# Optimization experiments

Hardware: AMD Instinct MI355X
Metric: run time of the kernel (lower is better)

Reference implementation:

```python
import jax, jax.numpy as jnp
import numpy as np

D_MODEL = 1024
N_HEADS = 16
HEAD_DIM = D_MODEL // N_HEADS
SCALE = HEAD_DIM ** -0.5
BATCH = 4
SEQ = 2048


def setup_inputs() -> dict:
    key = jax.random.key(0)
    k_x, k_wqkv, k_bqkv, k_wo, k_bo = jax.random.split(key, 5)
    x = jax.random.normal(k_x, (BATCH, SEQ, D_MODEL), dtype=jnp.float32)
    # causal mask: True = masked (matches torch masked_fill semantics)
    mask = jnp.triu(jnp.ones((SEQ, SEQ), dtype=bool), k=1)
    # Linear params (stored as [in, out] for x @ W)
    lim_qkv = (1.0 / D_MODEL) ** 0.5
    W_qkv = jax.random.uniform(k_wqkv, (D_MODEL, 3 * D_MODEL), jnp.float32, -lim_qkv, lim_qkv)
    b_qkv = jax.random.uniform(k_bqkv, (3 * D_MODEL,), jnp.float32, -lim_qkv, lim_qkv)
    W_out = jax.random.uniform(k_wo, (D_MODEL, D_MODEL), jnp.float32, -lim_qkv, lim_qkv)
    b_out = jax.random.uniform(k_bo, (D_MODEL,), jnp.float32, -lim_qkv, lim_qkv)
    return {"x": x, "mask": mask, "W_qkv": W_qkv, "b_qkv": b_qkv, "W_out": W_out, "b_out": b_out}


def reference(x, mask, W_qkv, b_qkv, W_out, b_out):
    b, s, d = x.shape
    qkv = x @ W_qkv + b_qkv                      # [b, s, 3d]
    qkv = qkv.reshape(b, s, 3, N_HEADS, HEAD_DIM)
    qkv = jnp.transpose(qkv, (2, 0, 3, 1, 4))    # [3, b, h, s, hd]
    q, k, v = qkv[0], qkv[1], qkv[2]
    scores = jnp.einsum('bhqd,bhkd->bhqk', q, k) * SCALE  # [b, h, s, s]
    scores = jnp.where(mask[None, None, :, :], -jnp.inf, scores)
    weights = jax.nn.softmax(scores, axis=-1)
    out = jnp.einsum('bhqk,bhkd->bhqd', weights, v)       # [b, h, s, hd]
    out = jnp.transpose(out, (0, 2, 1, 3)).reshape(b, s, d)
    return out @ W_out + b_out
```

## Files before the change

kernel.cpp:

```cpp
#include <hip/hip_runtime.h>

#define BATCH 4
#define SEQ 2048
#define DM 1024
#define NH 16
#define SCALE 0.125f

typedef unsigned short ushort_t;
typedef short bf16x8 __attribute__((ext_vector_type(8)));
typedef float f32x4 __attribute__((ext_vector_type(4)));

__device__ __forceinline__ ushort_t f2bf(float f) {
    unsigned u = __float_as_uint(f);
    unsigned r = (u + 0x7FFFu + ((u >> 16) & 1u)) >> 16;
    return (ushort_t)r;
}

__device__ __forceinline__ unsigned cvtpk_bf16(float lo, float hi) {
    unsigned r;
    asm("v_cvt_pk_bf16_f32 %0, %1, %2" : "=v"(r) : "v"(lo), "v"(hi));
    return r;
}

__device__ __forceinline__ void glds16(const ushort_t* g, ushort_t* l) {
    __builtin_amdgcn_global_load_lds(
        (const __attribute__((address_space(1))) unsigned*)g,
        (__attribute__((address_space(3))) unsigned*)l, 16, 0, 0);
}

__global__ void cast_f32_bf16(const float* __restrict__ in, ushort_t* __restrict__ out, int n) {
    int i = (blockIdx.x * blockDim.x + threadIdx.x) * 4;
    if (i < n) {
        float4 v = *(const float4*)(in + i);
        ushort4 o;
        o.x = f2bf(v.x); o.y = f2bf(v.y); o.z = f2bf(v.z); o.w = f2bf(v.w);
        *(ushort4*)(out + i) = o;
    }
}

__global__ void transpose_cast(const float* __restrict__ in, ushort_t* __restrict__ out,
                               int K, int N) {
    __shared__ float tile[32][33];
    int n0 = blockIdx.x * 32, k0 = blockIdx.y * 32;
    int x = threadIdx.x, y = threadIdx.y;
#pragma unroll
    for (int j = 0; j < 32; j += 8)
        tile[y + j][x] = in[(size_t)(k0 + y + j) * N + n0 + x];
    __syncthreads();
#pragma unroll
    for (int j = 0; j < 32; j += 8)
        out[(size_t)(n0 + y + j) * K + k0 + x] = f2bf(tile[x][y + j]);
}


__global__ __launch_bounds__(256) void gemm_qkv(
    const ushort_t* __restrict__ A, const ushort_t* __restrict__ Bt,
    const float* __restrict__ bias, ushort_t* __restrict__ qk,
    ushort_t* __restrict__ vt, int M, int N, int K) {
    __shared__ __attribute__((aligned(16))) ushort_t As[128 * 64];
    __shared__ __attribute__((aligned(16))) ushort_t Bs[128 * 64];
    const int tid = threadIdx.x;
    const int lane = tid & 63, wave = tid >> 6;
    const int l15 = lane & 15, l4 = lane >> 4;
    const int m0 = blockIdx.y * 128, n0 = blockIdx.x * 128;
    const int wr = (wave >> 1) * 64, wc = (wave & 1) * 64;
    const int r8 = lane >> 3;
    const int kch = (lane & 7) ^ r8;
    const ushort_t* gA = A + (size_t)(m0 + wave * 32 + r8) * K + kch * 8;
    const ushort_t* gB = Bt + (size_t)(n0 + wave * 32 + r8) * K + kch * 8;
    const int r7 = l15 & 7;

    f32x4 acc[4][4];
#pragma unroll
    for (int i = 0; i < 4; ++i)
#pragma unroll
        for (int j = 0; j < 4; ++j) acc[i][j] = (f32x4){0.f, 0.f, 0.f, 0.f};

    for (int k0 = 0; k0 < K; k0 += 64) {
#pragma unroll
        for (int c = 0; c < 4; ++c) {
            glds16(gA + k0 + (size_t)(c * 8) * K, &As[(wave * 32 + c * 8) * 64]);
            glds16(gB + k0 + (size_t)(c * 8) * K, &Bs[(wave * 32 + c * 8) * 64]);
        }
        __syncthreads();
#pragma unroll
        for (int kh = 0; kh < 2; ++kh) {
            const int ch = ((kh * 4 + l4) ^ r7) * 8;
            bf16x8 a[4], b[4];
#pragma unroll
            for (int i = 0; i < 4; ++i) {
                a[i] = *(const bf16x8*)&As[(wr + i * 16 + l15) * 64 + ch];
                b[i] = *(const bf16x8*)&Bs[(wc + i * 16 + l15) * 64 + ch];
            }
#pragma unroll
            for (int mi = 0; mi < 4; ++mi)
#pragma unroll
                for (int ni = 0; ni < 4; ++ni)
                    acc[mi][ni] = __builtin_amdgcn_mfma_f32_16x16x32_bf16(
                        a[mi], b[ni], acc[mi][ni], 0, 0, 0);
        }
        __syncthreads();
    }

    if (n0 < 2048) {
#pragma unroll
        for (int mi = 0; mi < 4; ++mi)
#pragma unroll
            for (int ni = 0; ni < 4; ++ni) {
                const int col = n0 + wc + ni * 16 + l15;
                const float bv = bias[col];
#pragma unroll
                for (int r = 0; r < 4; ++r) {
                    const int row = m0 + wr + mi * 16 + l4 * 4 + r;
                    qk[(size_t)row * 2048 + col] = f2bf(acc[mi][ni][r] + bv);
                }
            }
    } else {
#pragma unroll
        for (int mi = 0; mi < 4; ++mi)
#pragma unroll
            for (int ni = 0; ni < 4; ++ni) {
                const int hdg = n0 + wc + ni * 16 + l15 - 2048;
                const float bv = bias[2048 + hdg];
                const int row0 = m0 + wr + mi * 16 + l4 * 4;
                const int bb = row0 >> 11, s0 = row0 & 2047;
                ushort4 pk;
                pk.x = f2bf(acc[mi][ni][0] + bv);
                pk.y = f2bf(acc[mi][ni][1] + bv);
                pk.z = f2bf(acc[mi][ni][2] + bv);
                pk.w = f2bf(acc[mi][ni][3] + bv);
                *(ushort4*)&vt[((size_t)bb * 1024 + hdg) * 2048 + s0] = pk;
            }
    }
}

__global__ __launch_bounds__(256) void gemm_abt(
    const ushort_t* __restrict__ A, const ushort_t* __restrict__ Bt,
    const float* __restrict__ bias, float* __restrict__ Cout,
    int M, int N, int K) {
    __shared__ __attribute__((aligned(16))) ushort_t As[128 * 64];
    __shared__ __attribute__((aligned(16))) ushort_t Bs[128 * 64];
    const int tid = threadIdx.x;
    const int lane = tid & 63, wave = tid >> 6;
    const int l15 = lane & 15, l4 = lane >> 4;
    const int m0 = blockIdx.y * 128, n0 = blockIdx.x * 128;
    const int wr = (wave >> 1) * 64, wc = (wave & 1) * 64;
    const int r8 = lane >> 3;
    const int kch = (lane & 7) ^ r8;
    const ushort_t* gA = A + (size_t)(m0 + wave * 32 + r8) * K + kch * 8;
    const ushort_t* gB = Bt + (size_t)(n0 + wave * 32 + r8) * K + kch * 8;
    const int r7 = l15 & 7;

    f32x4 acc[4][4];
#pragma unroll
    for (int i = 0; i < 4; ++i)
#pragma unroll
        for (int j = 0; j < 4; ++j) acc[i][j] = (f32x4){0.f, 0.f, 0.f, 0.f};

    for (int k0 = 0; k0 < K; k0 += 64) {
#pragma unroll
        for (int c = 0; c < 4; ++c) {
            glds16(gA + k0 + (size_t)(c * 8) * K, &As[(wave * 32 + c * 8) * 64]);
            glds16(gB + k0 + (size_t)(c * 8) * K, &Bs[(wave * 32 + c * 8) * 64]);
        }
        __syncthreads();
#pragma unroll
        for (int kh = 0; kh < 2; ++kh) {
            const int ch = ((kh * 4 + l4) ^ r7) * 8;
            bf16x8 a[4], b[4];
#pragma unroll
            for (int i = 0; i < 4; ++i) {
                a[i] = *(const bf16x8*)&As[(wr + i * 16 + l15) * 64 + ch];
                b[i] = *(const bf16x8*)&Bs[(wc + i * 16 + l15) * 64 + ch];
            }
#pragma unroll
            for (int mi = 0; mi < 4; ++mi)
#pragma unroll
                for (int ni = 0; ni < 4; ++ni)
                    acc[mi][ni] = __builtin_amdgcn_mfma_f32_16x16x32_bf16(
                        a[mi], b[ni], acc[mi][ni], 0, 0, 0);
        }
        __syncthreads();
    }

#pragma unroll
    for (int mi = 0; mi < 4; ++mi)
#pragma unroll
        for (int ni = 0; ni < 4; ++ni)
#pragma unroll
            for (int r = 0; r < 4; ++r) {
                const int row = m0 + wr + mi * 16 + l4 * 4 + r;
                const int col = n0 + wc + ni * 16 + l15;
                Cout[(size_t)row * N + col] = acc[mi][ni][r] + bias[col];
            }
}

struct AState {
    bf16x8 q0, q1;
    f32x4 o[4];
    float m, l;
};

#define EXPC 0.18033688011112042f

template <bool MASK>
__device__ __forceinline__ void attn_tile(AState& S, const ushort_t* __restrict__ Ks,
                                          const ushort_t* __restrict__ Vt,
                                          ushort_t* __restrict__ Plw,
                                          int l15, int l4, int rel) {
    float p[16];
    float pmax = -INFINITY;
    __builtin_amdgcn_s_setprio(1);
#pragma unroll
    for (int kt = 0; kt < 4; ++kt) {
        const int row = kt * 16 + l15, r7 = row & 7;
        bf16x8 ak0 = *(const bf16x8*)&Ks[row * 64 + ((l4 ^ r7) * 8)];
        bf16x8 ak1 = *(const bf16x8*)&Ks[row * 64 + (((4 + l4) ^ r7) * 8)];
        f32x4 z = {0.f, 0.f, 0.f, 0.f};
        z = __builtin_amdgcn_mfma_f32_16x16x32_bf16(ak0, S.q0, z, 0, 0, 0);
        z = __builtin_amdgcn_mfma_f32_16x16x32_bf16(ak1, S.q1, z, 0, 0, 0);
#pragma unroll
        for (int r = 0; r < 4; ++r) {
            float v = z[r];
            if (MASK) v = (kt * 16 + l4 * 4 + r > rel) ? -INFINITY : v;
            p[kt * 4 + r] = v;
            pmax = fmaxf(pmax, v);
        }
    }
    __builtin_amdgcn_s_setprio(0);
    pmax = fmaxf(pmax, __shfl_xor(pmax, 16));
    pmax = fmaxf(pmax, __shfl_xor(pmax, 32));

    const bool defer = __all(pmax - S.m <= 64.f);
    const float mref = defer ? S.m : fmaxf(S.m, pmax);
    const float mC = mref * EXPC;
    float rsum = 0.f;
#pragma unroll
    for (int i = 0; i < 16; ++i) {
        p[i] = __builtin_exp2f(fmaf(p[i], EXPC, -mC));
        rsum += p[i];
    }
    rsum += __shfl_xor(rsum, 16);
    rsum += __shfl_xor(rsum, 32);
    if (defer) {
        S.l += rsum;
    } else {
        const float scl = __builtin_exp2f((S.m - mref) * EXPC);
        S.l = S.l * scl + rsum;
        S.m = mref;
        const float sc0 = __shfl(scl, l4 * 4 + 0);
        const float sc1 = __shfl(scl, l4 * 4 + 1);
        const float sc2 = __shfl(scl, l4 * 4 + 2);
        const float sc3 = __shfl(scl, l4 * 4 + 3);
#pragma unroll
        for (int dt = 0; dt < 4; ++dt) {
            S.o[dt][0] *= sc0; S.o[dt][1] *= sc1; S.o[dt][2] *= sc2; S.o[dt][3] *= sc3;
        }
    }

    const int pr7 = l15 & 7;
#pragma unroll
    for (int kt = 0; kt < 4; ++kt) {
        uint2 w;
        w.x = cvtpk_bf16(p[kt * 4 + 0], p[kt * 4 + 1]);
        w.y = cvtpk_bf16(p[kt * 4 + 2], p[kt * 4 + 3]);
        *(uint2*)&Plw[l15 * 64 + ((kt * 16 + l4 * 4) ^ (pr7 << 3))] = w;
    }

    bf16x8 pa0 = *(const bf16x8*)&Plw[l15 * 64 + ((l4 ^ pr7) * 8)];
    bf16x8 pa1 = *(const bf16x8*)&Plw[l15 * 64 + (((4 + l4) ^ pr7) * 8)];
    __builtin_amdgcn_s_setprio(1);
#pragma unroll
    for (int dt = 0; dt < 4; ++dt) {
        const int d = dt * 16 + l15, r7 = d & 7;
        bf16x8 bv0 = *(const bf16x8*)&Vt[d * 64 + ((l4 ^ r7) * 8)];
        bf16x8 bv1 = *(const bf16x8*)&Vt[d * 64 + (((4 + l4) ^ r7) * 8)];
        S.o[dt] = __builtin_amdgcn_mfma_f32_16x16x32_bf16(pa0, bv0, S.o[dt], 0, 0, 0);
        S.o[dt] = __builtin_amdgcn_mfma_f32_16x16x32_bf16(pa1, bv1, S.o[dt], 0, 0, 0);
    }
    __builtin_amdgcn_s_setprio(0);
}

__device__ __forceinline__ void process_qblock(
    int bq, const ushort_t* __restrict__ qk, ushort_t* __restrict__ out,
    size_t rowbase, int h, int wave, int l15, int l4,
    const ushort_t* gk, const ushort_t* gvt,
    ushort_t* Ks0, ushort_t* Ks1, ushort_t* Vt0, ushort_t* Vt1, ushort_t* Plw) {
    const int qbase = bq * 64 + wave * 16;

    AState S;
    {
        const ushort_t* qp = qk + (rowbase + qbase + l15) * 2048 + h * 64 + l4 * 8;
        S.q0 = *(const bf16x8*)qp;
        S.q1 = *(const bf16x8*)(qp + 32);
    }
#pragma unroll
    for (int i = 0; i < 4; ++i) S.o[i] = (f32x4){0.f, 0.f, 0.f, 0.f};
    S.m = -INFINITY;
    S.l = 0.f;

    glds16(gk, &Ks0[(wave * 16) * 64]);
    glds16(gk + (size_t)8 * 2048, &Ks0[(wave * 16 + 8) * 64]);
    glds16(gvt, &Vt0[(wave * 16) * 64]);
    glds16(gvt + (size_t)8 * 2048, &Vt0[(wave * 16 + 8) * 64]);
    __syncthreads();

    const int nt = bq + 1;
    for (int t = 0; t < nt; ++t) {
        ushort_t* Kc = (t & 1) ? Ks1 : Ks0;
        ushort_t* Vc = (t & 1) ? Vt1 : Vt0;
        ushort_t* Kn = (t & 1) ? Ks0 : Ks1;
        ushort_t* Vn = (t & 1) ? Vt0 : Vt1;
        if (t + 1 < nt) {
            const size_t koff = (size_t)(t + 1) * 64 * 2048;
            glds16(gk + koff, &Kn[(wave * 16) * 64]);
            glds16(gk + koff + (size_t)8 * 2048, &Kn[(wave * 16 + 8) * 64]);
            const size_t voff = (size_t)(t + 1) * 64;
            glds16(gvt + voff, &Vn[(wave * 16) * 64]);
            glds16(gvt + voff + (size_t)8 * 2048, &Vn[(wave * 16 + 8) * 64]);
        }
        if (t == bq)
            attn_tile<true>(S, Kc, Vc, Plw, l15, l4, wave * 16 + l15);
        else
            attn_tile<false>(S, Kc, Vc, Plw, l15, l4, 0);
        __syncthreads();
    }

    const float li0 = __shfl(S.l, l4 * 4 + 0);
    const float li1 = __shfl(S.l, l4 * 4 + 1);
    const float li2 = __shfl(S.l, l4 * 4 + 2);
    const float li3 = __shfl(S.l, l4 * 4 + 3);
#pragma unroll
    for (int r = 0; r < 4; ++r) {
        const int qr = qbase + l4 * 4 + r;
        const float li = (r == 0) ? li0 : (r == 1) ? li1 : (r == 2) ? li2 : li3;
        ushort_t* op = out + (rowbase + qr) * DM + h * 64 + l15;
#pragma unroll
        for (int dt = 0; dt < 4; ++dt)
            op[dt * 16] = f2bf(S.o[dt][r] / li);
    }
}

__global__ __launch_bounds__(256, 4) void attn_kernel(const ushort_t* __restrict__ qk,
                                                      const ushort_t* __restrict__ vt,
                                                      ushort_t* __restrict__ out) {
    __shared__ __attribute__((aligned(16))) ushort_t Ks[2][64 * 64];
    __shared__ __attribute__((aligned(16))) ushort_t Vt[2][64 * 64];
    __shared__ __attribute__((aligned(16))) ushort_t Pl[4][16 * 64];
    const int tid = threadIdx.x;
    const int wave = tid >> 6, lane = tid & 63;
    const int l15 = lane & 15, l4 = lane >> 4;
    const int bh = blockIdx.x;
    const int b = bh >> 4, h = bh & 15;
    const int pair = blockIdx.y;
    const size_t rowbase = (size_t)b * SEQ;

    const int krow = lane >> 3;
    const int kch = (lane & 7) ^ krow;
    const ushort_t* gk = qk + (rowbase + wave * 16 + krow) * 2048 + 1024 + h * 64 + kch * 8;
    const ushort_t* gvt = vt + ((size_t)b * 1024 + h * 64 + wave * 16 + krow) * 2048 + kch * 8;

    process_qblock(31 - pair, qk, out, rowbase, h, wave, l15, l4,
                   gk, gvt, Ks[0], Ks[1], Vt[0], Vt[1], Pl[wave]);
    process_qblock(pair, qk, out, rowbase, h, wave, l15, l4,
                   gk, gvt, Ks[0], Ks[1], Vt[0], Vt[1], Pl[wave]);
}

extern "C" void kernel_launch(void* const* d_in, const int* in_sizes, int n_in,
                              void* d_out, int out_size, void* d_ws, size_t ws_size,
                              hipStream_t stream) {
    const float* x     = (const float*)d_in[0];
    const float* W_qkv = (const float*)d_in[2];
    const float* b_qkv = (const float*)d_in[3];
    const float* W_out = (const float*)d_in[4];
    const float* b_out = (const float*)d_in[5];
    float* out = (float*)d_out;

    char* ws = (char*)d_ws;
    ushort_t* xb    = (ushort_t*)(ws);
    ushort_t* WqkvT = (ushort_t*)(ws + 16777216);
    ushort_t* WoutT = (ushort_t*)(ws + 23068672);
    ushort_t* qk    = (ushort_t*)(ws + 25165824);
    ushort_t* vt    = (ushort_t*)(ws + 58720256);
    ushort_t* attn  = (ushort_t*)(ws + 75497472);

    const int nx = BATCH * SEQ * DM;
    cast_f32_bf16<<<nx / (256 * 4), 256, 0, stream>>>(x, xb, nx);
    transpose_cast<<<dim3(3 * DM / 32, DM / 32), dim3(32, 8), 0, stream>>>(W_qkv, WqkvT, DM, 3 * DM);
    transpose_cast<<<dim3(DM / 32, DM / 32), dim3(32, 8), 0, stream>>>(W_out, WoutT, DM, DM);

    gemm_qkv<<<dim3(3 * DM / 128, BATCH * SEQ / 128), 256, 0, stream>>>(
        xb, WqkvT, b_qkv, qk, vt, BATCH * SEQ, 3 * DM, DM);

    attn_kernel<<<dim3(BATCH * NH, SEQ / 128), 256, 0, stream>>>(qk, vt, attn);

    gemm_abt<<<dim3(DM / 128, BATCH * SEQ / 128), 256, 0, stream>>>(
        attn, WoutT, b_out, out, BATCH * SEQ, DM, DM);
}
```

Before: 286.8 us.

## Process 32 query rows per wave to reuse K/V tiles across two states

Each wave now handles two 16-row query groups (128-row query blocks per workgroup), so every K and V fragment read from LDS feeds two sets of MFMAs, halving K/V global and LDS traffic per query. The softmax also defers the cross-lane row-sum reduction until the final store and only reduces the max when a rescale is needed. The grid shrinks to 8 blocks per head with launch bounds lowered to 2, trading occupancy and register pressure for the added reuse.

```diff
diff --git a/kernel.cpp b/kernel.cpp
--- a/kernel.cpp
+++ b/kernel.cpp
@@ -5,6 +5,7 @@
 #define DM 1024
 #define NH 16
 #define SCALE 0.125f
+#define EXPC 0.18033688011112042f
 
 typedef unsigned short ushort_t;
 typedef short bf16x8 __attribute__((ext_vector_type(8)));
@@ -51,7 +52,6 @@
     for (int j = 0; j < 32; j += 8)
         out[(size_t)(n0 + y + j) * K + k0 + x] = f2bf(tile[x][y + j]);
 }
-
 
 __global__ __launch_bounds__(256) void gemm_qkv(
     const ushort_t* __restrict__ A, const ushort_t* __restrict__ Bt,
@@ -201,53 +201,27 @@
     float m, l;
 };
 
-#define EXPC 0.18033688011112042f
-
 template <bool MASK>
-__device__ __forceinline__ void attn_tile(AState& S, const ushort_t* __restrict__ Ks,
-                                          const ushort_t* __restrict__ Vt,
-                                          ushort_t* __restrict__ Plw,
-                                          int l15, int l4, int rel) {
+__device__ __forceinline__ void softmax_state(const f32x4* z, AState& S,
+                                              ushort_t* __restrict__ Plw,
+                                              int l15, int l4, int rel) {
     float p[16];
     float pmax = -INFINITY;
-    __builtin_amdgcn_s_setprio(1);
-#pragma unroll
-    for (int kt = 0; kt < 4; ++kt) {
-        const int row = kt * 16 + l15, r7 = row & 7;
-        bf16x8 ak0 = *(const bf16x8*)&Ks[row * 64 + ((l4 ^ r7) * 8)];
-        bf16x8 ak1 = *(const bf16x8*)&Ks[row * 64 + (((4 + l4) ^ r7) * 8)];
-        f32x4 z = {0.f, 0.f, 0.f, 0.f};
-        z = __builtin_amdgcn_mfma_f32_16x16x32_bf16(ak0, S.q0, z, 0, 0, 0);
-        z = __builtin_amdgcn_mfma_f32_16x16x32_bf16(ak1, S.q1, z, 0, 0, 0);
+#pragma unroll
+    for (int kt = 0; kt < 4; ++kt)
 #pragma unroll
         for (int r = 0; r < 4; ++r) {
-            float v = z[r];
+            float v = z[kt][r];
             if (MASK) v = (kt * 16 + l4 * 4 + r > rel) ? -INFINITY : v;
             p[kt * 4 + r] = v;
             pmax = fmaxf(pmax, v);
         }
-    }
-    __builtin_amdgcn_s_setprio(0);
-    pmax = fmaxf(pmax, __shfl_xor(pmax, 16));
-    pmax = fmaxf(pmax, __shfl_xor(pmax, 32));
-
-    const bool defer = __all(pmax - S.m <= 64.f);
-    const float mref = defer ? S.m : fmaxf(S.m, pmax);
-    const float mC = mref * EXPC;
-    float rsum = 0.f;
-#pragma unroll
-    for (int i = 0; i < 16; ++i) {
-        p[i] = __builtin_exp2f(fmaf(p[i], EXPC, -mC));
-        rsum += p[i];
-    }
-    rsum += __shfl_xor(rsum, 16);
-    rsum += __shfl_xor(rsum, 32);
-    if (defer) {
-        S.l += rsum;
-    } else {
-        const float scl = __builtin_exp2f((S.m - mref) * EXPC);
-        S.l = S.l * scl + rsum;
-        S.m = mref;
+    if (!__all(pmax - S.m <= 64.f)) {
+        pmax = fmaxf(pmax, __shfl_xor(pmax, 16));
+        pmax = fmaxf(pmax, __shfl_xor(pmax, 32));
+        const float mnew = fmaxf(S.m, pmax);
+        const float scl = __builtin_exp2f((S.m - mnew) * EXPC);
+        S.l *= scl;
         const float sc0 = __shfl(scl, l4 * 4 + 0);
         const float sc1 = __shfl(scl, l4 * 4 + 1);
         const float sc2 = __shfl(scl, l4 * 4 + 2);
@@ -256,8 +230,16 @@
         for (int dt = 0; dt < 4; ++dt) {
             S.o[dt][0] *= sc0; S.o[dt][1] *= sc1; S.o[dt][2] *= sc2; S.o[dt][3] *= sc3;
         }
-    }
-
+        S.m = mnew;
+    }
+    const float mC = S.m * EXPC;
+    float rsum = 0.f;
+#pragma unroll
+    for (int i = 0; i < 16; ++i) {
+        p[i] = __builtin_exp2f(fmaf(p[i], EXPC, -mC));
+        rsum += p[i];
+    }
+    S.l += rsum;
     const int pr7 = l15 & 7;
 #pragma unroll
     for (int kt = 0; kt < 4; ++kt) {
@@ -266,70 +248,64 @@
         w.y = cvtpk_bf16(p[kt * 4 + 2], p[kt * 4 + 3]);
         *(uint2*)&Plw[l15 * 64 + ((kt * 16 + l4 * 4) ^ (pr7 << 3))] = w;
     }
-
-    bf16x8 pa0 = *(const bf16x8*)&Plw[l15 * 64 + ((l4 ^ pr7) * 8)];
-    bf16x8 pa1 = *(const bf16x8*)&Plw[l15 * 64 + (((4 + l4) ^ pr7) * 8)];
+}
+
+template <bool MASK>
+__device__ __forceinline__ void tile2(const ushort_t* __restrict__ Ksb,
+                                      const ushort_t* __restrict__ Vtb,
+                                      ushort_t* __restrict__ PlA,
+                                      ushort_t* __restrict__ PlB,
+                                      AState& SA, AState& SB,
+                                      int l15, int l4, int relA, int relB) {
+    f32x4 zA[4], zB[4];
+    __builtin_amdgcn_s_setprio(1);
+#pragma unroll
+    for (int kt = 0; kt < 4; ++kt) {
+        const int row = kt * 16 + l15, r7 = row & 7;
+        bf16x8 ak0 = *(const bf16x8*)&Ksb[row * 64 + ((l4 ^ r7) * 8)];
+        bf16x8 ak1 = *(const bf16x8*)&Ksb[row * 64 + (((4 + l4) ^ r7) * 8)];
+        f32x4 z = {0.f, 0.f, 0.f, 0.f};
+        z = __builtin_amdgcn_mfma_f32_16x16x32_bf16(ak0, SA.q0, z, 0, 0, 0);
+        z = __builtin_amdgcn_mfma_f32_16x16x32_bf16(ak1, SA.q1, z, 0, 0, 0);
+        zA[kt] = z;
+        f32x4 y = {0.f, 0.f, 0.f, 0.f};
+        y = __builtin_amdgcn_mfma_f32_16x16x32_bf16(ak0, SB.q0, y, 0, 0, 0);
+        y = __builtin_amdgcn_mfma_f32_16x16x32_bf16(ak1, SB.q1, y, 0, 0, 0);
+        zB[kt] = y;
+    }
+    __builtin_amdgcn_s_setprio(0);
+
+    softmax_state<MASK>(zA, SA, PlA, l15, l4, relA);
+    softmax_state<MASK>(zB, SB, PlB, l15, l4, relB);
+
+    const int pr7 = l15 & 7;
+    bf16x8 paA0 = *(const bf16x8*)&PlA[l15 * 64 + ((l4 ^ pr7) * 8)];
+    bf16x8 paA1 = *(const bf16x8*)&PlA[l15 * 64 + (((4 + l4) ^ pr7) * 8)];
+    bf16x8 paB0 = *(const bf16x8*)&PlB[l15 * 64 + ((l4 ^ pr7) * 8)];
+    bf16x8 paB1 = *(const bf16x8*)&PlB[l15 * 64 + (((4 + l4) ^ pr7) * 8)];
     __builtin_amdgcn_s_setprio(1);
 #pragma unroll
     for (int dt = 0; dt < 4; ++dt) {
         const int d = dt * 16 + l15, r7 = d & 7;
-        bf16x8 bv0 = *(const bf16x8*)&Vt[d * 64 + ((l4 ^ r7) * 8)];
-        bf16x8 bv1 = *(const bf16x8*)&Vt[d * 64 + (((4 + l4) ^ r7) * 8)];
-        S.o[dt] = __builtin_amdgcn_mfma_f32_16x16x32_bf16(pa0, bv0, S.o[dt], 0, 0, 0);
-        S.o[dt] = __builtin_amdgcn_mfma_f32_16x16x32_bf16(pa1, bv1, S.o[dt], 0, 0, 0);
+        bf16x8 bv0 = *(const bf16x8*)&Vtb[d * 64 + ((l4 ^ r7) * 8)];
+        bf16x8 bv1 = *(const bf16x8*)&Vtb[d * 64 + (((4 + l4) ^ r7) * 8)];
+        SA.o[dt] = __builtin_amdgcn_mfma_f32_16x16x32_bf16(paA0, bv0, SA.o[dt], 0, 0, 0);
+        SA.o[dt] = __builtin_amdgcn_mfma_f32_16x16x32_bf16(paA1, bv1, SA.o[dt], 0, 0, 0);
+        SB.o[dt] = __builtin_amdgcn_mfma_f32_16x16x32_bf16(paB0, bv0, SB.o[dt], 0, 0, 0);
+        SB.o[dt] = __builtin_amdgcn_mfma_f32_16x16x32_bf16(paB1, bv1, SB.o[dt], 0, 0, 0);
     }
     __builtin_amdgcn_s_setprio(0);
 }
 
-__device__ __forceinline__ void process_qblock(
-    int bq, const ushort_t* __restrict__ qk, ushort_t* __restrict__ out,
-    size_t rowbase, int h, int wave, int l15, int l4,
-    const ushort_t* gk, const ushort_t* gvt,
-    ushort_t* Ks0, ushort_t* Ks1, ushort_t* Vt0, ushort_t* Vt1, ushort_t* Plw) {
-    const int qbase = bq * 64 + wave * 16;
-
-    AState S;
-    {
-        const ushort_t* qp = qk + (rowbase + qbase + l15) * 2048 + h * 64 + l4 * 8;
-        S.q0 = *(const bf16x8*)qp;
-        S.q1 = *(const bf16x8*)(qp + 32);
-    }
-#pragma unroll
-    for (int i = 0; i < 4; ++i) S.o[i] = (f32x4){0.f, 0.f, 0.f, 0.f};
-    S.m = -INFINITY;
-    S.l = 0.f;
-
-    glds16(gk, &Ks0[(wave * 16) * 64]);
-    glds16(gk + (size_t)8 * 2048, &Ks0[(wave * 16 + 8) * 64]);
-    glds16(gvt, &Vt0[(wave * 16) * 64]);
-    glds16(gvt + (size_t)8 * 2048, &Vt0[(wave * 16 + 8) * 64]);
-    __syncthreads();
-
-    const int nt = bq + 1;
-    for (int t = 0; t < nt; ++t) {
-        ushort_t* Kc = (t & 1) ? Ks1 : Ks0;
-        ushort_t* Vc = (t & 1) ? Vt1 : Vt0;
-        ushort_t* Kn = (t & 1) ? Ks0 : Ks1;
-        ushort_t* Vn = (t & 1) ? Vt0 : Vt1;
-        if (t + 1 < nt) {
-            const size_t koff = (size_t)(t + 1) * 64 * 2048;
-            glds16(gk + koff, &Kn[(wave * 16) * 64]);
-            glds16(gk + koff + (size_t)8 * 2048, &Kn[(wave * 16 + 8) * 64]);
-            const size_t voff = (size_t)(t + 1) * 64;
-            glds16(gvt + voff, &Vn[(wave * 16) * 64]);
-            glds16(gvt + voff + (size_t)8 * 2048, &Vn[(wave * 16 + 8) * 64]);
-        }
-        if (t == bq)
-            attn_tile<true>(S, Kc, Vc, Plw, l15, l4, wave * 16 + l15);
-        else
-            attn_tile<false>(S, Kc, Vc, Plw, l15, l4, 0);
-        __syncthreads();
-    }
-
-    const float li0 = __shfl(S.l, l4 * 4 + 0);
-    const float li1 = __shfl(S.l, l4 * 4 + 1);
-    const float li2 = __shfl(S.l, l4 * 4 + 2);
-    const float li3 = __shfl(S.l, l4 * 4 + 3);
+__device__ __forceinline__ void attn_store(const AState& S, ushort_t* out, size_t rowbase,
+                                           int qbase, int h, int l15, int l4) {
+    float lt = S.l;
+    lt += __shfl_xor(lt, 16);
+    lt += __shfl_xor(lt, 32);
+    const float li0 = __shfl(lt, l4 * 4 + 0);
+    const float li1 = __shfl(lt, l4 * 4 + 1);
+    const float li2 = __shfl(lt, l4 * 4 + 2);
+    const float li3 = __shfl(lt, l4 * 4 + 3);
 #pragma unroll
     for (int r = 0; r < 4; ++r) {
         const int qr = qbase + l4 * 4 + r;
@@ -341,12 +317,12 @@
     }
 }
 
-__global__ __launch_bounds__(256, 4) void attn_kernel(const ushort_t* __restrict__ qk,
+__global__ __launch_bounds__(256, 2) void attn_kernel(const ushort_t* __restrict__ qk,
                                                       const ushort_t* __restrict__ vt,
                                                       ushort_t* __restrict__ out) {
     __shared__ __attribute__((aligned(16))) ushort_t Ks[2][64 * 64];
     __shared__ __attribute__((aligned(16))) ushort_t Vt[2][64 * 64];
-    __shared__ __attribute__((aligned(16))) ushort_t Pl[4][16 * 64];
+    __shared__ __attribute__((aligned(16))) ushort_t Pl[8][16 * 64];
     const int tid = threadIdx.x;
     const int wave = tid >> 6, lane = tid & 63;
     const int l15 = lane & 15, l4 = lane >> 4;
@@ -359,11 +335,76 @@
     const int kch = (lane & 7) ^ krow;
     const ushort_t* gk = qk + (rowbase + wave * 16 + krow) * 2048 + 1024 + h * 64 + kch * 8;
     const ushort_t* gvt = vt + ((size_t)b * 1024 + h * 64 + wave * 16 + krow) * 2048 + kch * 8;
-
-    process_qblock(31 - pair, qk, out, rowbase, h, wave, l15, l4,
-                   gk, gvt, Ks[0], Ks[1], Vt[0], Vt[1], Pl[wave]);
-    process_qblock(pair, qk, out, rowbase, h, wave, l15, l4,
-                   gk, gvt, Ks[0], Ks[1], Vt[0], Vt[1], Pl[wave]);
+    ushort_t* KsW0 = &Ks[0][(wave * 16) * 64];
+    ushort_t* KsW1 = &Ks[1][(wave * 16) * 64];
+    ushort_t* VtW0 = &Vt[0][(wave * 16) * 64];
+    ushort_t* VtW1 = &Vt[1][(wave * 16) * 64];
+    ushort_t* PlA = Pl[wave * 2];
+    ushort_t* PlB = Pl[wave * 2 + 1];
+
+#pragma unroll 1
+    for (int half = 0; half < 2; ++half) {
+        const int bq = half ? pair : (15 - pair);
+        const int qsA = bq * 128 + wave * 32;
+        const int qsB = qsA + 16;
+        const int nt = 2 * bq + 2;
+
+        AState SA, SB;
+        {
+            const ushort_t* qp = qk + (rowbase + qsA + l15) * 2048 + h * 64 + l4 * 8;
+            SA.q0 = *(const bf16x8*)qp;
+            SA.q1 = *(const bf16x8*)(qp + 32);
+            const ushort_t* qp2 = qp + (size_t)16 * 2048;
+            SB.q0 = *(const bf16x8*)qp2;
+            SB.q1 = *(const bf16x8*)(qp2 + 32);
+        }
+#pragma unroll
+        for (int i = 0; i < 4; ++i) {
+            SA.o[i] = (f32x4){0.f, 0.f, 0.f, 0.f};
+            SB.o[i] = (f32x4){0.f, 0.f, 0.f, 0.f};
+        }
+        SA.m = -INFINITY; SA.l = 0.f;
+        SB.m = -INFINITY; SB.l = 0.f;
+
+        glds16(gk, KsW0);
+        glds16(gk + (size_t)8 * 2048, KsW0 + 8 * 64);
+        glds16(gvt, VtW0);
+        glds16(gvt + (size_t)8 * 2048, VtW0 + 8 * 64);
+        __syncthreads();
+
+        const ushort_t* gks = gk + (size_t)64 * 2048;
+        const ushort_t* gvs = gvt + 64;
+        int t = 0;
+        for (; t + 2 < nt; t += 2) {
+            glds16(gks, KsW1);
+            glds16(gks + (size_t)8 * 2048, KsW1 + 8 * 64);
+            glds16(gvs, VtW1);
+            glds16(gvs + (size_t)8 * 2048, VtW1 + 8 * 64);
+            gks += (size_t)64 * 2048; gvs += 64;
+            tile2<false>(Ks[0], Vt[0], PlA, PlB, SA, SB, l15, l4, 0, 0);
+            __syncthreads();
+            glds16(gks, KsW0);
+            glds16(gks + (size_t)8 * 2048, KsW0 + 8 * 64);
+            glds16(gvs, VtW0);
+            glds16(gvs + (size_t)8 * 2048, VtW0 + 8 * 64);
+            gks += (size_t)64 * 2048; gvs += 64;
+            tile2<false>(Ks[1], Vt[1], PlA, PlB, SA, SB, l15, l4, 0, 0);
+            __syncthreads();
+        }
+        glds16(gks, KsW1);
+        glds16(gks + (size_t)8 * 2048, KsW1 + 8 * 64);
+        glds16(gvs, VtW1);
+        glds16(gvs + (size_t)8 * 2048, VtW1 + 8 * 64);
+        tile2<true>(Ks[0], Vt[0], PlA, PlB, SA, SB, l15, l4,
+                    qsA + l15 - (nt - 2) * 64, qsB + l15 - (nt - 2) * 64);
+        __syncthreads();
+        tile2<true>(Ks[1], Vt[1], PlA, PlB, SA, SB, l15, l4,
+                    qsA + l15 - (nt - 1) * 64, qsB + l15 - (nt - 1) * 64);
+
+        attn_store(SA, out, rowbase, qsA, h, l15, l4);
+        attn_store(SB, out, rowbase, qsB, h, l15, l4);
+        __syncthreads();
+    }
 }
 
 extern "C" void kernel_launch(void* const* d_in, const int* in_sizes, int n_in,
@@ -392,7 +433,7 @@
     gemm_qkv<<<dim3(3 * DM / 128, BATCH * SEQ / 128), 256, 0, stream>>>(
         xb, WqkvT, b_qkv, qk, vt, BATCH * SEQ, 3 * DM, DM);
 
-    attn_kernel<<<dim3(BATCH * NH, SEQ / 128), 256, 0, stream>>>(qk, vt, attn);
+    attn_kernel<<<dim3(BATCH * NH, 8), 256, 0, stream>>>(qk, vt, attn);
 
     gemm_abt<<<dim3(DM / 128, BATCH * SEQ / 128), 256, 0, stream>>>(
         attn, WoutT, b_out, out, BATCH * SEQ, DM, DM);
```

New measurement: 276.2 us. -3.7%, faster.
